# Kernel optimization log

Measured on AMD Instinct MI355X. Metric: run time of the kernel, lower is better.

The kernel has to match this reference:

```python
import jax, jax.numpy as jnp
import numpy as np

K = 2
LAMBDA_ALPHA = 1.0
LAMBDA_BETA = 0.5


def setup_inputs() -> dict:
    key = jax.random.key(0)
    ks = jax.random.split(key, 5)
    B, C, H, W = 32, 256, 56, 56
    R = 8
    hid = C // R
    return {
        "x": jax.random.normal(ks[0], (B, C, H, W), dtype=jnp.float32),
        "fc1_w": jax.random.normal(ks[1], (hid, C), dtype=jnp.float32) * 0.05,
        "fc1_b": jax.random.normal(ks[2], (hid,), dtype=jnp.float32) * 0.05,
        "fc2_w": jax.random.normal(ks[3], (K, 2 * C, hid), dtype=jnp.float32) * 0.05,
        "fc2_b": jax.random.normal(ks[4], (K, 2 * C), dtype=jnp.float32) * 0.05,
    }


def reference(x, fc1_w, fc1_b, fc2_w, fc2_b):
    # x: [B, C, H, W]
    k = fc2_w.shape[0]
    # squeeze-excite style context
    pooled = jnp.mean(x, axis=(2, 3))                         # [B, C]
    h = jax.nn.relu(pooled @ fc1_w.T + fc1_b)                 # [B, C/R]
    # k branch heads -> [k, B, 2C]
    delta = jnp.einsum("koh,bh->kbo", fc2_w, h) + fc2_b[:, None, :]
    delta = 2.0 * jax.nn.sigmoid(delta) - 1.0
    # de-interleave: even indices -> alpha, odd -> beta
    alpha = delta[..., 0::2]                                  # [k, B, C]
    beta = delta[..., 1::2]                                   # [k, B, C]
    init_alpha = jnp.zeros((k,), x.dtype).at[0].set(1.0)
    init_beta = jnp.zeros((k,), x.dtype).at[0].set(1.0)
    a = init_alpha[:, None, None] + LAMBDA_ALPHA * alpha      # [k, B, C]
    b = init_beta[:, None, None] + LAMBDA_BETA * beta         # [k, B, C]
    # broadcast affine per (k, batch, channel), then max over k
    out = x[None] * a[..., None, None] + b[..., None, None]   # [k, B, C, H, W]
    return jnp.max(out, axis=0)
```

## Files before the change

### kernel.cpp

```cpp
#include <hip/hip_runtime.h>
#include <math.h>

constexpr int B   = 32;
constexpr int C   = 256;
constexpr int HW  = 56 * 56;
constexpr int HW4 = HW / 4;
constexpr int HID = 32;
constexpr float LAMBDA_ALPHA = 1.0f;
constexpr float LAMBDA_BETA  = 0.5f;
constexpr int BDIM = 256;

__global__ __launch_bounds__(BDIM) void pool_kernel(const float* __restrict__ x,
                                                    float* __restrict__ pooled) {
    const int bc = blockIdx.x;
    const float4* x4 = reinterpret_cast<const float4*>(x) + (size_t)bc * HW4;

    float s = 0.0f;
    for (int t = threadIdx.x; t < HW4; t += BDIM) {
        float4 v = x4[t];
        s += (v.x + v.y) + (v.z + v.w);
    }
    for (int off = 32; off > 0; off >>= 1) s += __shfl_down(s, off, 64);

    __shared__ float wsum[BDIM / 64];
    const int lane = threadIdx.x & 63;
    const int wid  = threadIdx.x >> 6;
    if (lane == 0) wsum[wid] = s;
    __syncthreads();
    if (threadIdx.x == 0) {
        float tot = wsum[0] + wsum[1] + wsum[2] + wsum[3];
        pooled[bc] = tot * (1.0f / (float)HW);
    }
}

__global__ __launch_bounds__(BDIM) void fc1_kernel(const float* __restrict__ pooled,
                                                   const float* __restrict__ fc1_w,
                                                   const float* __restrict__ fc1_b,
                                                   float* __restrict__ h) {
    for (int i = threadIdx.x; i < B * HID; i += BDIM) {
        const int b  = i >> 5;
        const int hh = i & (HID - 1);
        const float4* pp = reinterpret_cast<const float4*>(pooled + b * C);
        const float4* pw = reinterpret_cast<const float4*>(fc1_w + hh * C);
        float acc = fc1_b[hh];
        #pragma unroll
        for (int q = 0; q < C / 4; ++q) {
            float4 p = pp[q], w = pw[q];
            acc = fmaf(p.x, w.x, fmaf(p.y, w.y, fmaf(p.z, w.z, fmaf(p.w, w.w, acc))));
        }
        h[i] = fmaxf(acc, 0.0f);
    }
}

__global__ __launch_bounds__(BDIM) void apply_kernel(const float* __restrict__ x,
                                                     const float* __restrict__ h,
                                                     const float* __restrict__ fc2_w,
                                                     const float* __restrict__ fc2_b,
                                                     float* __restrict__ out) {
    const int bc = blockIdx.x;
    const int b  = bc >> 8;
    const int c  = bc & (C - 1);

    const float4* h4 = reinterpret_cast<const float4*>(h + b * HID);
    float cf[4];
    #pragma unroll
    for (int k = 0; k < 2; ++k) {
        #pragma unroll
        for (int e = 0; e < 2; ++e) {
            const int o = 2 * c + e;
            const float4* w4 = reinterpret_cast<const float4*>(
                fc2_w + (size_t)(k * 2 * C + o) * HID);
            float acc = fc2_b[k * 2 * C + o];
            #pragma unroll
            for (int q = 0; q < HID / 4; ++q) {
                float4 w = w4[q], hv = h4[q];
                acc = fmaf(w.x, hv.x, fmaf(w.y, hv.y, fmaf(w.z, hv.z, fmaf(w.w, hv.w, acc))));
            }
            const float d = 2.0f / (1.0f + expf(-acc)) - 1.0f;
            cf[k * 2 + e] = ((k == 0) ? 1.0f : 0.0f) +
                            ((e == 0) ? LAMBDA_ALPHA : LAMBDA_BETA) * d;
        }
    }

    const float4* x4 = reinterpret_cast<const float4*>(x) + (size_t)bc * HW4;
    float4*       o4 = reinterpret_cast<float4*>(out) + (size_t)bc * HW4;
    for (int t = threadIdx.x; t < HW4; t += BDIM) {
        float4 v = x4[t];
        float4 r;
        r.x = fmaxf(fmaf(v.x, cf[0], cf[1]), fmaf(v.x, cf[2], cf[3]));
        r.y = fmaxf(fmaf(v.y, cf[0], cf[1]), fmaf(v.y, cf[2], cf[3]));
        r.z = fmaxf(fmaf(v.z, cf[0], cf[1]), fmaf(v.z, cf[2], cf[3]));
        r.w = fmaxf(fmaf(v.w, cf[0], cf[1]), fmaf(v.w, cf[2], cf[3]));
        o4[t] = r;
    }
}

extern "C" void kernel_launch(void* const* d_in, const int* in_sizes, int n_in,
                              void* d_out, int out_size, void* d_ws, size_t ws_size,
                              hipStream_t stream) {
    const float* x     = (const float*)d_in[0];
    const float* fc1_w = (const float*)d_in[1];
    const float* fc1_b = (const float*)d_in[2];
    const float* fc2_w = (const float*)d_in[3];
    const float* fc2_b = (const float*)d_in[4];
    float* out = (float*)d_out;

    float* pooled = (float*)d_ws;
    float* h      = pooled + (size_t)B * C;

    pool_kernel<<<B * C, BDIM, 0, stream>>>(x, pooled);
    fc1_kernel<<<1, BDIM, 0, stream>>>(pooled, fc1_w, fc1_b, h);
    apply_kernel<<<B * C, BDIM, 0, stream>>>(x, h, fc2_w, fc2_b, out);
}
```

Baseline: 230.6 us.

## Fuse pool, fc1 and apply into one cooperative persistent kernel

Replaces three kernel launches with a single cooperative kernel of 1024 blocks, each handling 8 (batch, channel) planes, using grid-wide syncs between pooling, the fc1 layer and the per-channel affine/max apply. The fc1 work is spread over 32 blocks instead of one, and fc2 coefficients are computed once per plane into shared memory rather than redundantly. This is meant to remove launch gaps and the single-block fc1 serialization, and may let the second read of x hit in cache. It adds two grid barriers and requires all blocks to be co-resident.

Result: slower. 398.2 us (+72.7%).

```diff
diff --git a/kernel.cpp b/kernel.cpp
--- a/kernel.cpp
+++ b/kernel.cpp
@@ -1,5 +1,8 @@
 #include <hip/hip_runtime.h>
+#include <hip/hip_cooperative_groups.h>
 #include <math.h>
+
+namespace cg = cooperative_groups;
 
 constexpr int B   = 32;
 constexpr int C   = 256;
@@ -9,89 +12,99 @@
 constexpr float LAMBDA_ALPHA = 1.0f;
 constexpr float LAMBDA_BETA  = 0.5f;
 constexpr int BDIM = 256;
+constexpr int GRID = 1024;
+constexpr int PPB  = (B * C) / GRID;
 
-__global__ __launch_bounds__(BDIM) void pool_kernel(const float* __restrict__ x,
-                                                    float* __restrict__ pooled) {
-    const int bc = blockIdx.x;
-    const float4* x4 = reinterpret_cast<const float4*>(x) + (size_t)bc * HW4;
-
-    float s = 0.0f;
-    for (int t = threadIdx.x; t < HW4; t += BDIM) {
-        float4 v = x4[t];
-        s += (v.x + v.y) + (v.z + v.w);
-    }
-    for (int off = 32; off > 0; off >>= 1) s += __shfl_down(s, off, 64);
+__global__ __launch_bounds__(BDIM, 4) void fused_kernel(
+    const float* __restrict__ x,
+    const float* __restrict__ fc1_w, const float* __restrict__ fc1_b,
+    const float* __restrict__ fc2_w, const float* __restrict__ fc2_b,
+    float* __restrict__ out,
+    float* __restrict__ pooled,
+    float* __restrict__ h)
+{
+    cg::grid_group grid = cg::this_grid();
+    const int tid  = threadIdx.x;
+    const int lane = tid & 63;
+    const int wid  = tid >> 6;
+    const int base = blockIdx.x * PPB;
 
     __shared__ float wsum[BDIM / 64];
-    const int lane = threadIdx.x & 63;
-    const int wid  = threadIdx.x >> 6;
-    if (lane == 0) wsum[wid] = s;
-    __syncthreads();
-    if (threadIdx.x == 0) {
-        float tot = wsum[0] + wsum[1] + wsum[2] + wsum[3];
-        pooled[bc] = tot * (1.0f / (float)HW);
-    }
-}
+    __shared__ float scoef[PPB][4];
 
-__global__ __launch_bounds__(BDIM) void fc1_kernel(const float* __restrict__ pooled,
-                                                   const float* __restrict__ fc1_w,
-                                                   const float* __restrict__ fc1_b,
-                                                   float* __restrict__ h) {
-    for (int i = threadIdx.x; i < B * HID; i += BDIM) {
-        const int b  = i >> 5;
-        const int hh = i & (HID - 1);
-        const float4* pp = reinterpret_cast<const float4*>(pooled + b * C);
-        const float4* pw = reinterpret_cast<const float4*>(fc1_w + hh * C);
-        float acc = fc1_b[hh];
-        #pragma unroll
-        for (int q = 0; q < C / 4; ++q) {
-            float4 p = pp[q], w = pw[q];
-            acc = fmaf(p.x, w.x, fmaf(p.y, w.y, fmaf(p.z, w.z, fmaf(p.w, w.w, acc))));
+    for (int i = 0; i < PPB; ++i) {
+        const int bc = base + i;
+        const float4* x4 = reinterpret_cast<const float4*>(x) + (size_t)bc * HW4;
+        float s = 0.0f;
+        for (int t = tid; t < HW4; t += BDIM) {
+            float4 v = x4[t];
+            s += (v.x + v.y) + (v.z + v.w);
         }
-        h[i] = fmaxf(acc, 0.0f);
-    }
-}
-
-__global__ __launch_bounds__(BDIM) void apply_kernel(const float* __restrict__ x,
-                                                     const float* __restrict__ h,
-                                                     const float* __restrict__ fc2_w,
-                                                     const float* __restrict__ fc2_b,
-                                                     float* __restrict__ out) {
-    const int bc = blockIdx.x;
-    const int b  = bc >> 8;
-    const int c  = bc & (C - 1);
-
-    const float4* h4 = reinterpret_cast<const float4*>(h + b * HID);
-    float cf[4];
-    #pragma unroll
-    for (int k = 0; k < 2; ++k) {
-        #pragma unroll
-        for (int e = 0; e < 2; ++e) {
-            const int o = 2 * c + e;
-            const float4* w4 = reinterpret_cast<const float4*>(
-                fc2_w + (size_t)(k * 2 * C + o) * HID);
-            float acc = fc2_b[k * 2 * C + o];
-            #pragma unroll
-            for (int q = 0; q < HID / 4; ++q) {
-                float4 w = w4[q], hv = h4[q];
-                acc = fmaf(w.x, hv.x, fmaf(w.y, hv.y, fmaf(w.z, hv.z, fmaf(w.w, hv.w, acc))));
-            }
-            const float d = 2.0f / (1.0f + expf(-acc)) - 1.0f;
-            cf[k * 2 + e] = ((k == 0) ? 1.0f : 0.0f) +
-                            ((e == 0) ? LAMBDA_ALPHA : LAMBDA_BETA) * d;
-        }
+        for (int off = 32; off > 0; off >>= 1) s += __shfl_down(s, off, 64);
+        if (lane == 0) wsum[wid] = s;
+        __syncthreads();
+        if (tid == 0)
+            pooled[bc] = (wsum[0] + wsum[1] + wsum[2] + wsum[3]) * (1.0f / (float)HW);
+        __syncthreads();
     }
 
-    const float4* x4 = reinterpret_cast<const float4*>(x) + (size_t)bc * HW4;
-    float4*       o4 = reinterpret_cast<float4*>(out) + (size_t)bc * HW4;
-    for (int t = threadIdx.x; t < HW4; t += BDIM) {
-        float4 v = x4[t];
-        float4 r;
-        r.x = fmaxf(fmaf(v.x, cf[0], cf[1]), fmaf(v.x, cf[2], cf[3]));
-        r.y = fmaxf(fmaf(v.y, cf[0], cf[1]), fmaf(v.y, cf[2], cf[3]));
-        r.z = fmaxf(fmaf(v.z, cf[0], cf[1]), fmaf(v.z, cf[2], cf[3]));
-        r.w = fmaxf(fmaf(v.w, cf[0], cf[1]), fmaf(v.w, cf[2], cf[3]));
-        o4[t] = r;
+    grid.sync();
+
+    if (blockIdx.x < B) {
+        const int b  = blockIdx.x;
+        const int hh = tid >> 3;
+        const int sub = tid & 7;
+        const float* pp = pooled + b * C;
+        const float* pw = fc1_w + hh * C;
+        float acc = 0.0f;
+        #pragma unroll
+        for (int q = 0; q < C / 8; ++q) {
+            const int c = sub * (C / 8) + q;
+            acc = fmaf(pp[c], pw[c], acc);
+        }
+        acc += __shfl_down(acc, 4, 64);
+        acc += __shfl_down(acc, 2, 64);
+        acc += __shfl_down(acc, 1, 64);
+        if (sub == 0) h[b * HID + hh] = fmaxf(acc + fc1_b[hh], 0.0f);
+    }
+
+    grid.sync();
+
+    if (tid < PPB * 4) {
+        const int i   = tid >> 2;
+        const int idx = tid & 3;
+        const int bc  = base + i;
+        const int b   = bc >> 8;
+        const int c   = bc & (C - 1);
+        const int k   = idx >> 1;
+        const int e   = idx & 1;
+        const int o   = 2 * c + e;
+        const float* w2 = fc2_w + (size_t)(k * 2 * C + o) * HID;
+        const float* hp = h + b * HID;
+        float acc = fc2_b[k * 2 * C + o];
+        #pragma unroll
+        for (int q = 0; q < HID; ++q) acc = fmaf(w2[q], hp[q], acc);
+        const float d = 2.0f / (1.0f + expf(-acc)) - 1.0f;
+        scoef[i][idx] = ((k == 0) ? 1.0f : 0.0f) +
+                        ((e == 0) ? LAMBDA_ALPHA : LAMBDA_BETA) * d;
+    }
+    __syncthreads();
+
+    for (int i = 0; i < PPB; ++i) {
+        const int bc = base + i;
+        const float a0 = scoef[i][0], b0 = scoef[i][1];
+        const float a1 = scoef[i][2], b1 = scoef[i][3];
+        const float4* x4 = reinterpret_cast<const float4*>(x) + (size_t)bc * HW4;
+        float4*       o4 = reinterpret_cast<float4*>(out) + (size_t)bc * HW4;
+        for (int t = tid; t < HW4; t += BDIM) {
+            float4 v = x4[t];
+            float4 r;
+            r.x = fmaxf(fmaf(v.x, a0, b0), fmaf(v.x, a1, b1));
+            r.y = fmaxf(fmaf(v.y, a0, b0), fmaf(v.y, a1, b1));
+            r.z = fmaxf(fmaf(v.z, a0, b0), fmaf(v.z, a1, b1));
+            r.w = fmaxf(fmaf(v.w, a0, b0), fmaf(v.w, a1, b1));
+            o4[t] = r;
+        }
     }
 }
 
@@ -108,7 +121,8 @@
     float* pooled = (float*)d_ws;
     float* h      = pooled + (size_t)B * C;
 
-    pool_kernel<<<B * C, BDIM, 0, stream>>>(x, pooled);
-    fc1_kernel<<<1, BDIM, 0, stream>>>(pooled, fc1_w, fc1_b, h);
-    apply_kernel<<<B * C, BDIM, 0, stream>>>(x, h, fc2_w, fc2_b, out);
+    void* args[] = { (void*)&x, (void*)&fc1_w, (void*)&fc1_b, (void*)&fc2_w,
+                     (void*)&fc2_b, (void*)&out, (void*)&pooled, (void*)&h };
+    hipLaunchCooperativeKernel((void*)fused_kernel, dim3(GRID), dim3(BDIM),
+                               args, 0, stream);
 }
```

## Map one wavefront per channel and parallelize fc1 across batch blocks

Applied to the files above, without the earlier changes.

Pool and apply kernels now assign one 64-lane wavefront per (batch, channel) plane instead of a whole 256-thread block. Each wavefront walks its plane with a fully unrolled loop plus a tail, and the pool kernel drops the shared-memory cross-wave reduction and its barrier. The fc1 kernel moves from a single block to one block per batch, with 8 lanes per hidden unit and a shuffle reduction. The goal is to cut block scheduling and sync overhead and to spread the tiny fc1 step across the GPU, at the cost of fewer threads per plane and a larger unrolled body.

New measurement: 205.7 us. 10.8% less time.

```diff
diff --git a/kernel.cpp b/kernel.cpp
--- a/kernel.cpp
+++ b/kernel.cpp
@@ -9,47 +9,51 @@
 constexpr float LAMBDA_ALPHA = 1.0f;
 constexpr float LAMBDA_BETA  = 0.5f;
 constexpr int BDIM = 256;
+constexpr int WPB  = BDIM / 64;
+constexpr int FULL = HW4 / 64;
+constexpr int TAIL = HW4 - FULL * 64;
 
 __global__ __launch_bounds__(BDIM) void pool_kernel(const float* __restrict__ x,
                                                     float* __restrict__ pooled) {
-    const int bc = blockIdx.x;
+    const int lane = threadIdx.x & 63;
+    const int wid  = threadIdx.x >> 6;
+    const int bc   = blockIdx.x * WPB + wid;
     const float4* x4 = reinterpret_cast<const float4*>(x) + (size_t)bc * HW4;
 
     float s = 0.0f;
-    for (int t = threadIdx.x; t < HW4; t += BDIM) {
-        float4 v = x4[t];
+    #pragma unroll
+    for (int r = 0; r < FULL; ++r) {
+        float4 v = x4[r * 64 + lane];
+        s += (v.x + v.y) + (v.z + v.w);
+    }
+    if (lane < TAIL) {
+        float4 v = x4[FULL * 64 + lane];
         s += (v.x + v.y) + (v.z + v.w);
     }
     for (int off = 32; off > 0; off >>= 1) s += __shfl_down(s, off, 64);
-
-    __shared__ float wsum[BDIM / 64];
-    const int lane = threadIdx.x & 63;
-    const int wid  = threadIdx.x >> 6;
-    if (lane == 0) wsum[wid] = s;
-    __syncthreads();
-    if (threadIdx.x == 0) {
-        float tot = wsum[0] + wsum[1] + wsum[2] + wsum[3];
-        pooled[bc] = tot * (1.0f / (float)HW);
-    }
+    if (lane == 0) pooled[bc] = s * (1.0f / (float)HW);
 }
 
 __global__ __launch_bounds__(BDIM) void fc1_kernel(const float* __restrict__ pooled,
                                                    const float* __restrict__ fc1_w,
                                                    const float* __restrict__ fc1_b,
                                                    float* __restrict__ h) {
-    for (int i = threadIdx.x; i < B * HID; i += BDIM) {
-        const int b  = i >> 5;
-        const int hh = i & (HID - 1);
-        const float4* pp = reinterpret_cast<const float4*>(pooled + b * C);
-        const float4* pw = reinterpret_cast<const float4*>(fc1_w + hh * C);
-        float acc = fc1_b[hh];
-        #pragma unroll
-        for (int q = 0; q < C / 4; ++q) {
-            float4 p = pp[q], w = pw[q];
-            acc = fmaf(p.x, w.x, fmaf(p.y, w.y, fmaf(p.z, w.z, fmaf(p.w, w.w, acc))));
-        }
-        h[i] = fmaxf(acc, 0.0f);
+    const int b   = blockIdx.x;
+    const int tid = threadIdx.x;
+    const int hh  = tid >> 3;
+    const int sub = tid & 7;
+    const float* pp = pooled + b * C;
+    const float* pw = fc1_w + hh * C;
+    float acc = 0.0f;
+    #pragma unroll
+    for (int q = 0; q < C / 8; ++q) {
+        const int c = sub * (C / 8) + q;
+        acc = fmaf(pp[c], pw[c], acc);
     }
+    acc += __shfl_down(acc, 4, 64);
+    acc += __shfl_down(acc, 2, 64);
+    acc += __shfl_down(acc, 1, 64);
+    if (sub == 0) h[b * HID + hh] = fmaxf(acc + fc1_b[hh], 0.0f);
 }
 
 __global__ __launch_bounds__(BDIM) void apply_kernel(const float* __restrict__ x,
@@ -57,25 +61,23 @@
                                                      const float* __restrict__ fc2_w,
                                                      const float* __restrict__ fc2_b,
                                                      float* __restrict__ out) {
-    const int bc = blockIdx.x;
-    const int b  = bc >> 8;
-    const int c  = bc & (C - 1);
+    const int lane = threadIdx.x & 63;
+    const int wid  = threadIdx.x >> 6;
+    const int bc   = blockIdx.x * WPB + wid;
+    const int b    = bc >> 8;
+    const int c    = bc & (C - 1);
+    const float* hp = h + b * HID;
 
-    const float4* h4 = reinterpret_cast<const float4*>(h + b * HID);
     float cf[4];
     #pragma unroll
     for (int k = 0; k < 2; ++k) {
         #pragma unroll
         for (int e = 0; e < 2; ++e) {
             const int o = 2 * c + e;
-            const float4* w4 = reinterpret_cast<const float4*>(
-                fc2_w + (size_t)(k * 2 * C + o) * HID);
+            const float* w2 = fc2_w + (size_t)(k * 2 * C + o) * HID;
             float acc = fc2_b[k * 2 * C + o];
             #pragma unroll
-            for (int q = 0; q < HID / 4; ++q) {
-                float4 w = w4[q], hv = h4[q];
-                acc = fmaf(w.x, hv.x, fmaf(w.y, hv.y, fmaf(w.z, hv.z, fmaf(w.w, hv.w, acc))));
-            }
+            for (int q = 0; q < HID; ++q) acc = fmaf(w2[q], hp[q], acc);
             const float d = 2.0f / (1.0f + expf(-acc)) - 1.0f;
             cf[k * 2 + e] = ((k == 0) ? 1.0f : 0.0f) +
                             ((e == 0) ? LAMBDA_ALPHA : LAMBDA_BETA) * d;
@@ -84,14 +86,24 @@
 
     const float4* x4 = reinterpret_cast<const float4*>(x) + (size_t)bc * HW4;
     float4*       o4 = reinterpret_cast<float4*>(out) + (size_t)bc * HW4;
-    for (int t = threadIdx.x; t < HW4; t += BDIM) {
-        float4 v = x4[t];
-        float4 r;
-        r.x = fmaxf(fmaf(v.x, cf[0], cf[1]), fmaf(v.x, cf[2], cf[3]));
-        r.y = fmaxf(fmaf(v.y, cf[0], cf[1]), fmaf(v.y, cf[2], cf[3]));
-        r.z = fmaxf(fmaf(v.z, cf[0], cf[1]), fmaf(v.z, cf[2], cf[3]));
-        r.w = fmaxf(fmaf(v.w, cf[0], cf[1]), fmaf(v.w, cf[2], cf[3]));
-        o4[t] = r;
+    #pragma unroll
+    for (int r = 0; r < FULL; ++r) {
+        float4 v = x4[r * 64 + lane];
+        float4 rr;
+        rr.x = fmaxf(fmaf(v.x, cf[0], cf[1]), fmaf(v.x, cf[2], cf[3]));
+        rr.y = fmaxf(fmaf(v.y, cf[0], cf[1]), fmaf(v.y, cf[2], cf[3]));
+        rr.z = fmaxf(fmaf(v.z, cf[0], cf[1]), fmaf(v.z, cf[2], cf[3]));
+        rr.w = fmaxf(fmaf(v.w, cf[0], cf[1]), fmaf(v.w, cf[2], cf[3]));
+        o4[r * 64 + lane] = rr;
+    }
+    if (lane < TAIL) {
+        float4 v = x4[FULL * 64 + lane];
+        float4 rr;
+        rr.x = fmaxf(fmaf(v.x, cf[0], cf[1]), fmaf(v.x, cf[2], cf[3]));
+        rr.y = fmaxf(fmaf(v.y, cf[0], cf[1]), fmaf(v.y, cf[2], cf[3]));
+        rr.z = fmaxf(fmaf(v.z, cf[0], cf[1]), fmaf(v.z, cf[2], cf[3]));
+        rr.w = fmaxf(fmaf(v.w, cf[0], cf[1]), fmaf(v.w, cf[2], cf[3]));
+        o4[FULL * 64 + lane] = rr;
     }
 }
 
@@ -108,7 +120,7 @@
     float* pooled = (float*)d_ws;
     float* h      = pooled + (size_t)B * C;
 
-    pool_kernel<<<B * C, BDIM, 0, stream>>>(x, pooled);
-    fc1_kernel<<<1, BDIM, 0, stream>>>(pooled, fc1_w, fc1_b, h);
-    apply_kernel<<<B * C, BDIM, 0, stream>>>(x, h, fc2_w, fc2_b, out);
+    pool_kernel<<<(B * C) / WPB, BDIM, 0, stream>>>(x, pooled);
+    fc1_kernel<<<B, BDIM, 0, stream>>>(pooled, fc1_w, fc1_b, h);
+    apply_kernel<<<(B * C) / WPB, BDIM, 0, stream>>>(x, h, fc2_w, fc2_b, out);
 }
```
